# Performance work log

Hardware: AMD Instinct MI355X
Metric: run time of the kernel (lower is better)

## Reference

```python
import jax, jax.numpy as jnp
import numpy as np

EPS = 1e-8
WINDOW = 3      # config.router_window_size
TEMP = 1.0      # config.router_temp (> 0, so sqrt(D) fallback unused)
TOP_K = 2       # config.moe_top_k


def _routing_weights(x, prototypes):
    # L2-normalize router input per token (normalize_router_input=True)
    x = x / jnp.clip(jnp.linalg.norm(x, axis=-1, keepdims=True), EPS)
    # 'window' mode: causal moving average of size WINDOW along seq, with the
    # first token replicated WINDOW-1 times on the left (matches F.conv1d with
    # left pad of flat_input[:, :, [0]] and an averaging kernel).
    w = WINDOW
    padded = jnp.concatenate([jnp.repeat(x[:, :1], w - 1, axis=1), x], axis=1)  # [B, S+w-1, D]
    cs = jnp.concatenate(
        [jnp.zeros_like(padded[:, :1]), jnp.cumsum(padded, axis=1)], axis=1
    )  # [B, S+w, D]
    router_input = (cs[:, w:] - cs[:, :-w]) / w  # [B, S, D] moving mean
    # F.linear(router_input, prototypes): logits over experts
    logits = jnp.einsum('bsd,ed->bse', router_input, prototypes)  # [B, S, E]
    # softmax in float32 (F.softmax(..., dtype=torch.float))
    return jax.nn.softmax((logits / TEMP).astype(jnp.float32), axis=-1)


def setup_inputs() -> dict:
    key = jax.random.key(0)
    k1, k2 = jax.random.split(key)
    bs, sq, D, E = 8, 2048, 1024, 64
    x = jax.random.normal(k1, (bs, sq, D), dtype=jnp.float32)
    prototypes = jax.random.normal(k2, (E, D), dtype=jnp.float32) * 0.02
    attn_mask = jnp.ones((bs, sq), dtype=jnp.int32)
    return {"x": x, "prototypes": prototypes, "attn_mask": attn_mask}


def reference(x, prototypes, attn_mask):
    # attn_mask is all ones here; in 'window' mode it only feeds logging stats.
    routing_weights = _routing_weights(x, prototypes)          # [B, S, E]
    weights, modules = jax.lax.top_k(routing_weights, TOP_K)   # [B, S, K]
    weights = weights / weights.sum(axis=-1, keepdims=True)    # renormalize top-k
    return modules, weights
```

## Files before the change

kernel.cpp:

```cpp
#include <hip/hip_runtime.h>
#include <math.h>


#define BB 8
#define SS 2048
#define DD 1024
#define EE 64
#define EPSV 1e-8f

__global__ __launch_bounds__(256) void repack_proto(
    const float* __restrict__ proto, float* __restrict__ ptt) {
  const int gid = blockIdx.x * 256 + threadIdx.x;
  const int d = gid >> 6;
  const int e = gid & 63;
  ptt[gid] = proto[(size_t)e * DD + d];
}

__global__ __launch_bounds__(1024) void router_dots(
    const float* __restrict__ x, const float* __restrict__ ptt,
    float* __restrict__ dots) {
  __shared__ float SMEM[8960];

  const int tid  = threadIdx.x;
  const int lane = tid & 63;
  const int w    = __builtin_amdgcn_readfirstlane(tid >> 6);
  const int we   = w & 3;
  const int wk   = w >> 2;
  const int b    = blockIdx.x >> 5;
  const int s0   = (blockIdx.x & 31) * 64;

  const int gl = tid & 255;
  const int st = gl >> 2;
  const int sq = gl & 3;

  float* xtw = SMEM + wk * 2176;
  float* nqp = SMEM + 8704;

  const float* xsrow =
      x + ((size_t)b * SS + s0 + st) * DD + wk * 256 + sq * 4;
  const float* pr = ptt + (size_t)(wk * 256) * EE + we * 16;

  float4 acc0 = make_float4(0.f, 0.f, 0.f, 0.f);
  float4 acc1 = make_float4(0.f, 0.f, 0.f, 0.f);
  float4 acc2 = make_float4(0.f, 0.f, 0.f, 0.f);
  float4 acc3 = make_float4(0.f, 0.f, 0.f, 0.f);
  float q = 0.0f;

  {
    const float4 v = *(const float4*)(xsrow);
    float* d = xtw + (sq * 4) * 68 + st;
    d[0]   = v.x;
    d[68]  = v.y;
    d[136] = v.z;
    d[204] = v.w;
  }
  __syncthreads();

  for (int c = 0; c < 16; ++c) {
    const int buf = c & 1;
    float4 nv;
    if (c + 1 < 16) nv = *(const float4*)(xsrow + (c + 1) * 16);
    const float* xk_base = xtw + buf * 1088 + lane;
    const float* pp = pr + (size_t)(c * 16) * EE;
#pragma unroll
    for (int kk = 0; kk < 16; ++kk) {
      const float xk = xk_base[kk * 68];
      q += xk * xk;
      const float4 p0 = *(const float4*)(pp + kk * 64);
      const float4 p1 = *(const float4*)(pp + kk * 64 + 4);
      const float4 p2 = *(const float4*)(pp + kk * 64 + 8);
      const float4 p3 = *(const float4*)(pp + kk * 64 + 12);
      acc0.x += xk * p0.x; acc0.y += xk * p0.y;
      acc0.z += xk * p0.z; acc0.w += xk * p0.w;
      acc1.x += xk * p1.x; acc1.y += xk * p1.y;
      acc1.z += xk * p1.z; acc1.w += xk * p1.w;
      acc2.x += xk * p2.x; acc2.y += xk * p2.y;
      acc2.z += xk * p2.z; acc2.w += xk * p2.w;
      acc3.x += xk * p3.x; acc3.y += xk * p3.y;
      acc3.z += xk * p3.z; acc3.w += xk * p3.w;
    }
    if (c + 1 < 16) {
      float* d = xtw + (buf ^ 1) * 1088 + (sq * 4) * 68 + st;
      d[0]   = nv.x;
      d[68]  = nv.y;
      d[136] = nv.z;
      d[204] = nv.w;
    }
    __syncthreads();
  }

  if (we == 0) nqp[wk * 64 + lane] = q;

  float* B0 = SMEM;
  float* B1 = SMEM + 4096;

#define WRB(R)                                              \
  { float* p_ = (R) + we * 1024 + lane * 4;                 \
    *(float4*)(p_ + 0)   = acc0;                            \
    *(float4*)(p_ + 256) = acc1;                            \
    *(float4*)(p_ + 512) = acc2;                            \
    *(float4*)(p_ + 768) = acc3; }
#define ADDB(R)                                             \
  { const float* p_ = (R) + we * 1024 + lane * 4;           \
    const float4 t0 = *(const float4*)(p_ + 0);             \
    const float4 t1 = *(const float4*)(p_ + 256);           \
    const float4 t2 = *(const float4*)(p_ + 512);           \
    const float4 t3 = *(const float4*)(p_ + 768);           \
    acc0.x += t0.x; acc0.y += t0.y; acc0.z += t0.z; acc0.w += t0.w; \
    acc1.x += t1.x; acc1.y += t1.y; acc1.z += t1.z; acc1.w += t1.w; \
    acc2.x += t2.x; acc2.y += t2.y; acc2.z += t2.z; acc2.w += t2.w; \
    acc3.x += t3.x; acc3.y += t3.y; acc3.z += t3.z; acc3.w += t3.w; }

  __syncthreads();
  if (wk == 1) WRB(B0)
  if (wk == 3) WRB(B1)
  __syncthreads();
  if (wk == 0) ADDB(B0)
  if (wk == 2) ADDB(B1)
  __syncthreads();
  if (wk == 2) WRB(B0)
  __syncthreads();
  if (wk == 0) {
    ADDB(B0)
    const float qs = nqp[lane] + nqp[64 + lane] +
                     nqp[128 + lane] + nqp[192 + lane];
    const float inv = 1.0f / fmaxf(sqrtf(qs), EPSV);
    acc0.x *= inv; acc0.y *= inv; acc0.z *= inv; acc0.w *= inv;
    acc1.x *= inv; acc1.y *= inv; acc1.z *= inv; acc1.w *= inv;
    acc2.x *= inv; acc2.y *= inv; acc2.z *= inv; acc2.w *= inv;
    acc3.x *= inv; acc3.y *= inv; acc3.z *= inv; acc3.w *= inv;
    float* dp = dots + ((size_t)b * SS + s0 + lane) * EE + we * 16;
    *(float4*)(dp)      = acc0;
    *(float4*)(dp + 4)  = acc1;
    *(float4*)(dp + 8)  = acc2;
    *(float4*)(dp + 12) = acc3;
  }
}

#define T2UP(s, ei)                                            \
  if ((s) > v1) { v2 = v1; i2 = i1; v1 = (s); i1 = (ei); }     \
  else if ((s) > v2) { v2 = (s); i2 = (ei); }

__global__ __launch_bounds__(256) void router_top2(
    const float* __restrict__ dots, float* __restrict__ out) {
  const int gtid = blockIdx.x * 256 + threadIdx.x;
  const int tok  = gtid >> 3;
  const int h    = gtid & 7;
  const int b    = tok >> 11;
  const int sl   = tok & (SS - 1);
  const int r0   = (sl >= 2) ? sl - 2 : 0;
  const int r1   = (sl >= 1) ? sl - 1 : 0;

  const float* d0 = dots + ((size_t)b * SS + r0) * EE + h * 8;
  const float* d1 = dots + ((size_t)b * SS + r1) * EE + h * 8;
  const float* d2 = dots + ((size_t)b * SS + sl) * EE + h * 8;

  float v1 = -INFINITY, v2 = -INFINITY;
  int i1 = 0, i2 = 0;
#pragma unroll
  for (int qd = 0; qd < 2; ++qd) {
    const float4 a = *(const float4*)(d0 + qd * 4);
    const float4 c = *(const float4*)(d1 + qd * 4);
    const float4 e = *(const float4*)(d2 + qd * 4);
    const int e0 = h * 8 + qd * 4;
    float s;
    s = a.x + c.x + e.x; T2UP(s, e0 + 0)
    s = a.y + c.y + e.y; T2UP(s, e0 + 1)
    s = a.z + c.z + e.z; T2UP(s, e0 + 2)
    s = a.w + c.w + e.w; T2UP(s, e0 + 3)
  }

#pragma unroll
  for (int m = 1; m <= 4; m <<= 1) {
    const float ov1 = __shfl_xor(v1, m);
    const int   oi1 = __shfl_xor(i1, m);
    const float ov2 = __shfl_xor(v2, m);
    const int   oi2 = __shfl_xor(i2, m);
    const bool o_beats = (ov1 > v1) || (ov1 == v1 && oi1 < i1);
    if (o_beats) {
      const bool v1_beats_o2 = (v1 > ov2) || (v1 == ov2 && i1 < oi2);
      v2 = v1_beats_o2 ? v1 : ov2;
      i2 = v1_beats_o2 ? i1 : oi2;
      v1 = ov1;
      i1 = oi1;
    } else {
      const bool o1_beats_v2 = (ov1 > v2) || (ov1 == v2 && oi1 < i2);
      if (o1_beats_v2) { v2 = ov1; i2 = oi1; }
    }
  }

  if (h == 0) {
    const float ex = expf((v2 - v1) * (1.0f / 3.0f));
    const float w1 = 1.0f / (1.0f + ex);
    const size_t o = (size_t)tok * 2;
    *(float2*)(out + o) = make_float2((float)i1, (float)i2);
    *(float2*)(out + (size_t)BB * SS * 2 + o) = make_float2(w1, ex * w1);
  }
}

extern "C" void kernel_launch(void* const* d_in, const int* in_sizes, int n_in,
                              void* d_out, int out_size, void* d_ws, size_t ws_size,
                              hipStream_t stream) {
  const float* x     = (const float*)d_in[0];
  const float* proto = (const float*)d_in[1];
  float* out  = (float*)d_out;
  float* ptt  = (float*)d_ws;
  float* dots = (float*)((char*)d_ws + (512 << 10));

  repack_proto<<<dim3(256), dim3(256), 0, stream>>>(proto, ptt);
  router_dots<<<dim3(256), dim3(1024), 0, stream>>>(x, ptt, dots);
  router_top2<<<dim3(512), dim3(256), 0, stream>>>(dots, out);
}
```

Measured before the change: 129.7 us.

## Register-tile router dot products per wave with private LDS staging

Restructures router_dots so each of 8 waves owns a 128-wide slice of D and computes a full 64-token by 64-expert tile, with each lane holding an 8x8 register block. Both x and the transposed prototypes are staged in per-wave private LDS, so the main loop no longer needs block-wide barriers. The aim is more reuse per LDS read and fewer per-FMA loads than the previous one-token-per-lane layout. The cost is a deeper multi-step cross-wave reduction, higher register pressure, and half as many threads per block.

```diff
diff --git a/kernel.cpp b/kernel.cpp
--- a/kernel.cpp
+++ b/kernel.cpp
@@ -7,6 +7,11 @@
 #define DD 1024
 #define EE 64
 #define EPSV 1e-8f
+
+#define FMA4(A, s, P) \
+  A.x += (s) * (P).x; A.y += (s) * (P).y; A.z += (s) * (P).z; A.w += (s) * (P).w;
+
+#define SUMSQ4(v) ((v).x * (v).x + (v).y * (v).y + (v).z * (v).z + (v).w * (v).w)
 
 __global__ __launch_bounds__(256) void repack_proto(
     const float* __restrict__ proto, float* __restrict__ ptt) {
@@ -16,124 +21,163 @@
   ptt[gid] = proto[(size_t)e * DD + d];
 }
 
-__global__ __launch_bounds__(1024) void router_dots(
+__global__ __launch_bounds__(512) void router_dots(
     const float* __restrict__ x, const float* __restrict__ ptt,
     float* __restrict__ dots) {
-  __shared__ float SMEM[8960];
+  __shared__ float SMEM[9216];
 
   const int tid  = threadIdx.x;
   const int lane = tid & 63;
   const int w    = __builtin_amdgcn_readfirstlane(tid >> 6);
-  const int we   = w & 3;
-  const int wk   = w >> 2;
+  const int eg   = lane & 7;
+  const int tg   = lane >> 3;
   const int b    = blockIdx.x >> 5;
   const int s0   = (blockIdx.x & 31) * 64;
 
-  const int gl = tid & 255;
-  const int st = gl >> 2;
-  const int sq = gl & 3;
-
-  float* xtw = SMEM + wk * 2176;
+  float* xtw = SMEM + w * 544;
+  float* ptw = SMEM + 4352 + w * 512;
   float* nqp = SMEM + 8704;
 
-  const float* xsrow =
-      x + ((size_t)b * SS + s0 + st) * DD + wk * 256 + sq * 4;
-  const float* pr = ptt + (size_t)(wk * 256) * EE + we * 16;
-
-  float4 acc0 = make_float4(0.f, 0.f, 0.f, 0.f);
-  float4 acc1 = make_float4(0.f, 0.f, 0.f, 0.f);
-  float4 acc2 = make_float4(0.f, 0.f, 0.f, 0.f);
-  float4 acc3 = make_float4(0.f, 0.f, 0.f, 0.f);
+  const int kbase = w * 128;
+  const float* xsrow = x + ((size_t)b * SS + s0 + lane) * DD + kbase;
+  const float* psrow = ptt + (size_t)kbase * EE + lane * 4;
+
+  float4 accA0[4], accA1[4], accB0[4], accB1[4];
+#pragma unroll
+  for (int i = 0; i < 4; ++i) {
+    accA0[i] = make_float4(0.f, 0.f, 0.f, 0.f);
+    accA1[i] = make_float4(0.f, 0.f, 0.f, 0.f);
+    accB0[i] = make_float4(0.f, 0.f, 0.f, 0.f);
+    accB1[i] = make_float4(0.f, 0.f, 0.f, 0.f);
+  }
   float q = 0.0f;
 
   {
-    const float4 v = *(const float4*)(xsrow);
-    float* d = xtw + (sq * 4) * 68 + st;
-    d[0]   = v.x;
-    d[68]  = v.y;
-    d[136] = v.z;
-    d[204] = v.w;
-  }
-  __syncthreads();
+    const float4 v0 = *(const float4*)(xsrow);
+    const float4 v1 = *(const float4*)(xsrow + 4);
+    const float4 r0 = *(const float4*)(psrow);
+    const float4 r1 = *(const float4*)(psrow + 256);
+    q += SUMSQ4(v0) + SUMSQ4(v1);
+    float* d = xtw + lane;
+    d[0]   = v0.x; d[68]  = v0.y; d[136] = v0.z; d[204] = v0.w;
+    d[272] = v1.x; d[340] = v1.y; d[408] = v1.z; d[476] = v1.w;
+    *(float4*)(ptw + lane * 4)       = r0;
+    *(float4*)(ptw + 256 + lane * 4) = r1;
+  }
+
+  const float* xc = xtw + tg * 8;
+  const float* pc = ptw + eg * 8;
 
   for (int c = 0; c < 16; ++c) {
-    const int buf = c & 1;
-    float4 nv;
-    if (c + 1 < 16) nv = *(const float4*)(xsrow + (c + 1) * 16);
-    const float* xk_base = xtw + buf * 1088 + lane;
-    const float* pp = pr + (size_t)(c * 16) * EE;
-#pragma unroll
-    for (int kk = 0; kk < 16; ++kk) {
-      const float xk = xk_base[kk * 68];
-      q += xk * xk;
-      const float4 p0 = *(const float4*)(pp + kk * 64);
-      const float4 p1 = *(const float4*)(pp + kk * 64 + 4);
-      const float4 p2 = *(const float4*)(pp + kk * 64 + 8);
-      const float4 p3 = *(const float4*)(pp + kk * 64 + 12);
-      acc0.x += xk * p0.x; acc0.y += xk * p0.y;
-      acc0.z += xk * p0.z; acc0.w += xk * p0.w;
-      acc1.x += xk * p1.x; acc1.y += xk * p1.y;
-      acc1.z += xk * p1.z; acc1.w += xk * p1.w;
-      acc2.x += xk * p2.x; acc2.y += xk * p2.y;
-      acc2.z += xk * p2.z; acc2.w += xk * p2.w;
-      acc3.x += xk * p3.x; acc3.y += xk * p3.y;
-      acc3.z += xk * p3.z; acc3.w += xk * p3.w;
-    }
+    float4 v0, v1, r0, r1;
     if (c + 1 < 16) {
-      float* d = xtw + (buf ^ 1) * 1088 + (sq * 4) * 68 + st;
-      d[0]   = nv.x;
-      d[68]  = nv.y;
-      d[136] = nv.z;
-      d[204] = nv.w;
-    }
-    __syncthreads();
-  }
-
-  if (we == 0) nqp[wk * 64 + lane] = q;
+      v0 = *(const float4*)(xsrow + (c + 1) * 8);
+      v1 = *(const float4*)(xsrow + (c + 1) * 8 + 4);
+      r0 = *(const float4*)(psrow + (c + 1) * 512);
+      r1 = *(const float4*)(psrow + (c + 1) * 512 + 256);
+    }
+#pragma unroll
+    for (int kk = 0; kk < 8; ++kk) {
+      const float4 xfA = *(const float4*)(xc + kk * 68);
+      const float4 xfB = *(const float4*)(xc + kk * 68 + 4);
+      const float4 p0  = *(const float4*)(pc + kk * 64);
+      const float4 p1  = *(const float4*)(pc + kk * 64 + 4);
+      FMA4(accA0[0], xfA.x, p0) FMA4(accA1[0], xfA.x, p1)
+      FMA4(accA0[1], xfA.y, p0) FMA4(accA1[1], xfA.y, p1)
+      FMA4(accA0[2], xfA.z, p0) FMA4(accA1[2], xfA.z, p1)
+      FMA4(accA0[3], xfA.w, p0) FMA4(accA1[3], xfA.w, p1)
+      FMA4(accB0[0], xfB.x, p0) FMA4(accB1[0], xfB.x, p1)
+      FMA4(accB0[1], xfB.y, p0) FMA4(accB1[1], xfB.y, p1)
+      FMA4(accB0[2], xfB.z, p0) FMA4(accB1[2], xfB.z, p1)
+      FMA4(accB0[3], xfB.w, p0) FMA4(accB1[3], xfB.w, p1)
+    }
+    if (c + 1 < 16) {
+      q += SUMSQ4(v0) + SUMSQ4(v1);
+      float* d = xtw + lane;
+      d[0]   = v0.x; d[68]  = v0.y; d[136] = v0.z; d[204] = v0.w;
+      d[272] = v1.x; d[340] = v1.y; d[408] = v1.z; d[476] = v1.w;
+      *(float4*)(ptw + lane * 4)       = r0;
+      *(float4*)(ptw + 256 + lane * 4) = r1;
+    }
+  }
+
+  nqp[w * 64 + lane] = q;
 
   float* B0 = SMEM;
-  float* B1 = SMEM + 4096;
-
-#define WRB(R)                                              \
-  { float* p_ = (R) + we * 1024 + lane * 4;                 \
-    *(float4*)(p_ + 0)   = acc0;                            \
-    *(float4*)(p_ + 256) = acc1;                            \
-    *(float4*)(p_ + 512) = acc2;                            \
-    *(float4*)(p_ + 768) = acc3; }
-#define ADDB(R)                                             \
-  { const float* p_ = (R) + we * 1024 + lane * 4;           \
-    const float4 t0 = *(const float4*)(p_ + 0);             \
-    const float4 t1 = *(const float4*)(p_ + 256);           \
-    const float4 t2 = *(const float4*)(p_ + 512);           \
-    const float4 t3 = *(const float4*)(p_ + 768);           \
-    acc0.x += t0.x; acc0.y += t0.y; acc0.z += t0.z; acc0.w += t0.w; \
-    acc1.x += t1.x; acc1.y += t1.y; acc1.z += t1.z; acc1.w += t1.w; \
-    acc2.x += t2.x; acc2.y += t2.y; acc2.z += t2.z; acc2.w += t2.w; \
-    acc3.x += t3.x; acc3.y += t3.y; acc3.z += t3.z; acc3.w += t3.w; }
-
-  __syncthreads();
-  if (wk == 1) WRB(B0)
-  if (wk == 3) WRB(B1)
-  __syncthreads();
-  if (wk == 0) ADDB(B0)
-  if (wk == 2) ADDB(B1)
-  __syncthreads();
-  if (wk == 2) WRB(B0)
-  __syncthreads();
-  if (wk == 0) {
+  float* B1 = SMEM + 4352;
+
+#define WRB(R)                                                        \
+  { _Pragma("unroll") for (int i = 0; i < 4; ++i) {                   \
+      float* pA_ = (R) + (tg * 8 + i) * 68 + eg * 8;                  \
+      float* pB_ = (R) + (tg * 8 + 4 + i) * 68 + eg * 8;              \
+      *(float4*)(pA_)     = accA0[i];                                 \
+      *(float4*)(pA_ + 4) = accA1[i];                                 \
+      *(float4*)(pB_)     = accB0[i];                                 \
+      *(float4*)(pB_ + 4) = accB1[i]; } }
+#define ADDB(R)                                                       \
+  { _Pragma("unroll") for (int i = 0; i < 4; ++i) {                   \
+      const float* pA_ = (R) + (tg * 8 + i) * 68 + eg * 8;            \
+      const float* pB_ = (R) + (tg * 8 + 4 + i) * 68 + eg * 8;        \
+      const float4 tA0 = *(const float4*)(pA_);                       \
+      const float4 tA1 = *(const float4*)(pA_ + 4);                   \
+      const float4 tB0 = *(const float4*)(pB_);                       \
+      const float4 tB1 = *(const float4*)(pB_ + 4);                   \
+      accA0[i].x += tA0.x; accA0[i].y += tA0.y;                       \
+      accA0[i].z += tA0.z; accA0[i].w += tA0.w;                       \
+      accA1[i].x += tA1.x; accA1[i].y += tA1.y;                       \
+      accA1[i].z += tA1.z; accA1[i].w += tA1.w;                       \
+      accB0[i].x += tB0.x; accB0[i].y += tB0.y;                       \
+      accB0[i].z += tB0.z; accB0[i].w += tB0.w;                       \
+      accB1[i].x += tB1.x; accB1[i].y += tB1.y;                       \
+      accB1[i].z += tB1.z; accB1[i].w += tB1.w; } }
+
+  __syncthreads();
+  if (w == 1) WRB(B0)
+  if (w == 5) WRB(B1)
+  __syncthreads();
+  if (w == 0) ADDB(B0)
+  if (w == 4) ADDB(B1)
+  __syncthreads();
+  if (w == 3) WRB(B0)
+  if (w == 7) WRB(B1)
+  __syncthreads();
+  if (w == 2) ADDB(B0)
+  if (w == 6) ADDB(B1)
+  __syncthreads();
+  if (w == 2) WRB(B0)
+  if (w == 6) WRB(B1)
+  __syncthreads();
+  if (w == 0) ADDB(B0)
+  if (w == 4) ADDB(B1)
+  __syncthreads();
+  if (w == 4) WRB(B0)
+  __syncthreads();
+  if (w == 0) {
     ADDB(B0)
-    const float qs = nqp[lane] + nqp[64 + lane] +
-                     nqp[128 + lane] + nqp[192 + lane];
-    const float inv = 1.0f / fmaxf(sqrtf(qs), EPSV);
-    acc0.x *= inv; acc0.y *= inv; acc0.z *= inv; acc0.w *= inv;
-    acc1.x *= inv; acc1.y *= inv; acc1.z *= inv; acc1.w *= inv;
-    acc2.x *= inv; acc2.y *= inv; acc2.z *= inv; acc2.w *= inv;
-    acc3.x *= inv; acc3.y *= inv; acc3.z *= inv; acc3.w *= inv;
-    float* dp = dots + ((size_t)b * SS + s0 + lane) * EE + we * 16;
-    *(float4*)(dp)      = acc0;
-    *(float4*)(dp + 4)  = acc1;
-    *(float4*)(dp + 8)  = acc2;
-    *(float4*)(dp + 12) = acc3;
+#pragma unroll
+    for (int i = 0; i < 4; ++i) {
+      const int rA = tg * 8 + i;
+      const int rB = rA + 4;
+      float qsA = 0.0f, qsB = 0.0f;
+#pragma unroll
+      for (int ww = 0; ww < 8; ++ww) {
+        qsA += nqp[ww * 64 + rA];
+        qsB += nqp[ww * 64 + rB];
+      }
+      const float invA = 1.0f / fmaxf(sqrtf(qsA), EPSV);
+      const float invB = 1.0f / fmaxf(sqrtf(qsB), EPSV);
+      float4 oA0 = accA0[i], oA1 = accA1[i], oB0 = accB0[i], oB1 = accB1[i];
+      oA0.x *= invA; oA0.y *= invA; oA0.z *= invA; oA0.w *= invA;
+      oA1.x *= invA; oA1.y *= invA; oA1.z *= invA; oA1.w *= invA;
+      oB0.x *= invB; oB0.y *= invB; oB0.z *= invB; oB0.w *= invB;
+      oB1.x *= invB; oB1.y *= invB; oB1.z *= invB; oB1.w *= invB;
+      float* dpA = dots + ((size_t)b * SS + s0 + rA) * EE + eg * 8;
+      float* dpB = dots + ((size_t)b * SS + s0 + rB) * EE + eg * 8;
+      *(float4*)(dpA)     = oA0;
+      *(float4*)(dpA + 4) = oA1;
+      *(float4*)(dpB)     = oB0;
+      *(float4*)(dpB + 4) = oB1;
+    }
   }
 }
 
@@ -208,6 +252,6 @@
   float* dots = (float*)((char*)d_ws + (512 << 10));
 
   repack_proto<<<dim3(256), dim3(256), 0, stream>>>(proto, ptt);
-  router_dots<<<dim3(256), dim3(1024), 0, stream>>>(x, ptt, dots);
+  router_dots<<<dim3(256), dim3(512), 0, stream>>>(x, ptt, dots);
   router_top2<<<dim3(512), dim3(256), 0, stream>>>(dots, out);
 }
```

Result: faster. 126.8 us (-2.2%).
